# Kernel optimization log

Measured on AMD Instinct MI355X. Metric: run time of the kernel, lower is better.

The kernel has to match this reference:

```python
import jax, jax.numpy as jnp
import numpy as np

K = 16
RADIUS = 1.0
N = 16384
SEQ = 8


def _knn(pc, k):
    """Brute-force kNN of pc against itself. pc: (1, n, 3).
    Returns (dist, idx) each (1, n, k), sorted ascending by distance,
    matching pointutils.knn semantics (Euclidean distance)."""
    x2 = jnp.sum(pc * pc, axis=-1)  # (1, n)
    # d2[b,i,j] = ||p_i - p_j||^2 via expansion; avoids (n,n,3) intermediate
    d2 = x2[:, :, None] + x2[:, None, :] - 2.0 * jnp.einsum('bnd,bmd->bnm', pc, pc)
    d2 = jnp.maximum(d2, 0.0)
    neg_d2, idx = jax.lax.top_k(-d2, k)  # k smallest distances
    dist = jnp.sqrt(jnp.maximum(-neg_d2, 0.0))
    return dist, idx


def setup_inputs() -> dict:
    key = jax.random.key(0)
    k1, k2, k3 = jax.random.split(key, 3)
    return {
        'pc_source': jax.random.normal(k1, (1, N, 3), dtype=jnp.float32),
        'pred_flow': jax.random.normal(k2, (SEQ, N, 3), dtype=jnp.float32),
        'weights': jax.random.uniform(k3, (N,), dtype=jnp.float32),
    }


def reference(pc_source, pred_flow, weights):
    # flow: (seq, 3, n)
    flow = jnp.transpose(pred_flow, (0, 2, 1))
    dist, idx = _knn(pc_source, K)  # (1, n, k)
    # replace out-of-radius neighbors with the nearest (self) index
    idx = jnp.where(dist > RADIUS, idx[:, :, 0:1], idx)
    idx = idx[0]  # (n, k); identical for all sequence steps
    # grouping_operation: gather neighbor flows -> (seq, 3, n, k)
    nn_flow = flow[:, :, idx]
    diff = flow[:, :, :, None] - nn_flow  # (seq, 3, n, k)
    # L2 norm over channel dim (loss_norm=2), safe at 0 (self-neighbor)
    sq = jnp.sum(diff * diff, axis=1)  # (seq, n, k)
    norm = jnp.where(sq > 0, jnp.sqrt(jnp.where(sq > 0, sq, 1.0)), 0.0)
    loss = norm.mean(axis=-1)  # (seq, n)
    loss = loss * weights[None, :]
    loss = loss.sum(axis=1)  # (seq,)
    wsum = weights.sum()
    loss = jnp.where(wsum > 0, loss / wsum, loss)
    return loss.mean()
```

## Files before the change

### kernel.cpp

```cpp
#include <hip/hip_runtime.h>
#include <math.h>

#define NPTS  16384
#define KNN   16
#define SEQV  8
#define NW    16
#define BATCH 8
#define CAPM  15
#define CAPR  1.001f
#define NBKT  256
#define BSCALE 56.8888f
#define HBLK  16

#define SLOT(arr, t, col) arr[(t) * 1024 + (col)]

#define WS_HIST   256
#define WS_STARTS (WS_HIST + NBKT * HBLK * 4)
#define WS_SORTED 18432

__device__ __forceinline__ unsigned umin_(unsigned a, unsigned b) { return a < b ? a : b; }
__device__ __forceinline__ unsigned umax_(unsigned a, unsigned b) { return a > b ? a : b; }

__device__ __forceinline__ int nbucket(float x) { return (int)fminf(x * BSCALE, 255.0f); }

__device__ __forceinline__ void merge_one(unsigned keys[KNN], unsigned kk) {
    if (kk < keys[KNN - 1]) {
#pragma unroll
        for (int u = 0; u < KNN; ++u) {
            unsigned lo = umin_(kk, keys[u]);
            kk = umax_(kk, keys[u]);
            keys[u] = lo;
        }
    }
}

__device__ __forceinline__ void merge16(unsigned k[KNN], const unsigned o[KNN]) {
    unsigned v[KNN];
#pragma unroll
    for (int i = 0; i < KNN; ++i) v[i] = umin_(k[i], o[KNN - 1 - i]);
#pragma unroll
    for (int d = 8; d >= 1; d >>= 1) {
#pragma unroll
        for (int i = 0; i < KNN; ++i) {
            if ((i & d) == 0) {
                unsigned lo = umin_(v[i], v[i + d]);
                unsigned hi = umax_(v[i], v[i + d]);
                v[i] = lo; v[i + d] = hi;
            }
        }
    }
#pragma unroll
    for (int i = 0; i < KNN; ++i) k[i] = v[i];
}

__device__ __forceinline__ void tree_load_merge(unsigned* uS, unsigned keys[KNN], int src) {
    unsigned o[KNN];
#pragma unroll
    for (int t = 0; t < KNN; ++t) o[t] = SLOT(uS, t, src);
    merge16(keys, o);
}

__global__ __launch_bounds__(1024) void hist_kernel(
    const float* __restrict__ pc, unsigned* __restrict__ hist)
{
    __shared__ unsigned h[NBKT];
    const int tid = threadIdx.x;
    if (tid < NBKT) h[tid] = 0u;
    __syncthreads();
    const int i = blockIdx.x * 1024 + tid;
    const float x = pc[3 * i + 0], y = pc[3 * i + 1], z = pc[3 * i + 2];
    const float n = sqrtf(fmaf(x, x, fmaf(y, y, z * z)));
    atomicAdd(&h[nbucket(n)], 1u);
    __syncthreads();
    if (tid < NBKT) hist[tid * HBLK + blockIdx.x] = h[tid];
}

__global__ __launch_bounds__(1024) void scatter_kernel(
    const float* __restrict__ pc, const unsigned* __restrict__ hist,
    unsigned* __restrict__ starts, float* __restrict__ accum,
    float4* __restrict__ sorted4)
{
    __shared__ unsigned sH[NBKT];
    __shared__ unsigned sBase[NBKT];
    __shared__ unsigned sCnt[NBKT];
    const int tid = threadIdx.x;
    const int b   = blockIdx.x;

    unsigned own = 0, pre = 0;
    if (tid < NBKT) {
        const unsigned* row = hist + tid * HBLK;
        unsigned s = 0, p = 0;
#pragma unroll
        for (int k = 0; k < HBLK; ++k) {
            const unsigned c = row[k];
            if (k < b) p += c;
            s += c;
        }
        own = s; pre = p;
        sH[tid] = s;
        sCnt[tid] = 0u;
    }
    __syncthreads();
    for (int off = 1; off < NBKT; off <<= 1) {
        unsigned a = 0u;
        if (tid < NBKT && tid >= off) a = sH[tid - off];
        __syncthreads();
        if (tid < NBKT) sH[tid] += a;
        __syncthreads();
    }
    if (tid < NBKT) {
        const unsigned excl = sH[tid] - own;
        sBase[tid] = excl + pre;
        if (b == 0) starts[tid] = excl;
    }
    if (b == 0 && tid == 0) starts[NBKT] = NPTS;
    if (b == 0 && tid < 8) ((unsigned*)accum)[tid] = 0u;
    __syncthreads();

    const int i = b * 1024 + tid;
    const float x = pc[3 * i + 0], y = pc[3 * i + 1], z = pc[3 * i + 2];
    const float n = sqrtf(fmaf(x, x, fmaf(y, y, z * z)));
    const int bin = nbucket(n);
    const unsigned rank = atomicAdd(&sCnt[bin], 1u);
    sorted4[sBase[bin] + rank] = make_float4(x, y, z, __uint_as_float((unsigned)i));
    if (b == 0 && tid < 8)
        sorted4[NPTS + tid] = make_float4(1e18f, 1e18f, 1e18f, __uint_as_float(0u));
}

__global__ __launch_bounds__(1024, 4) void mega_kernel(
    const float4* __restrict__ sorted, const unsigned* __restrict__ starts,
    const float* __restrict__ flow, const float* __restrict__ wts,
    float* __restrict__ accum, float* __restrict__ out)
{
    __shared__ unsigned uS[1024 * 16];
    float* sred = (float*)&uS[15 * 1024 + 1000];
    float* sTau = (float*)&uS[16320];

    const int tid  = threadIdx.x;
    const int lane = tid & 63;
    const int wv   = __builtin_amdgcn_readfirstlane(tid >> 6);
    const int is   = blockIdx.x * 64 + lane;

    const float4 q4 = sorted[is];
    const float qx = q4.x, qy = q4.y, qz = q4.z;
    const unsigned iorig = __float_as_uint(q4.w);
    const float q2 = fmaf(qx, qx, fmaf(qy, qy, qz * qz));
    const float analytic = 0.19072f * exp2f(0.480898f * q2);
    const float tau0 = fminf(analytic, CAPR);

    const float nq = sqrtf(q2);
    float nmin = nq, nmax = nq;
#pragma unroll
    for (int off = 32; off > 0; off >>= 1) {
        nmin = fminf(nmin, __shfl_xor(nmin, off));
        nmax = fmaxf(nmax, __shfl_xor(nmax, off));
    }
    const float r0 = sqrtf(fminf(0.19072f * exp2f(0.480898f * nmax * nmax), CAPR));
    const int blo = nbucket(fmaxf(nmin - r0, 0.0f));
    const int bhi = nbucket(nmax + r0);
    const int W0  = __builtin_amdgcn_readfirstlane((int)starts[blo]);
    const int W1  = __builtin_amdgcn_readfirstlane((int)starts[bhi + 1]);
    const int nbt = (W1 - W0 + 7) >> 3;

    unsigned keys[KNN];
#pragma unroll
    for (int t = 0; t < KNN; ++t) keys[t] = 0xFFFFFFFFu;
    int cnt = 0;
    unsigned* buf = &uS[tid * CAPM];

    {
        float tauT = tau0;
        const float4* cb = sorted + W0;
        float4 A[BATCH], Bv[BATCH];

        auto procT = [&](const float4* C) {
#pragma unroll
            for (int q = 0; q < BATCH; ++q) {
                const float4 c = C[q];
                float dx = qx - c.x, dy = qy - c.y, dz = qz - c.z;
                float d2 = fmaf(dx, dx, fmaf(dy, dy, dz * dz));
                bool acc = d2 <= tauT;
                if (__any(acc)) {
                    if (acc) {
                        buf[cnt] = (__float_as_uint(d2) & 0xFFFFC000u)
                                 | __float_as_uint(c.w);
                        ++cnt;
                    }
                    if (cnt >= CAPM - 1) {
#pragma unroll 1
                        for (int t = 0; t < cnt; ++t) merge_one(keys, buf[t]);
                        cnt = 0;
                        float d16n = __uint_as_float(keys[KNN - 1] & 0xFFFFC000u);
                        tauT = fminf(tauT, fmaf(d16n, 1.0002f, 1e-6f));
                    }
                }
            }
        };

        int g = wv;
        bool hA = (g < nbt);
        if (hA) { const float4* bp = cb + 8 * g;
#pragma unroll
            for (int q = 0; q < BATCH; ++q) A[q] = bp[q]; }
        while (hA) {
            int g2 = g + 64;
            bool hB = (g2 < nbt);
            if (hB) { const float4* bp = cb + 8 * g2;
#pragma unroll
                for (int q = 0; q < BATCH; ++q) Bv[q] = bp[q]; }
            procT(A);
            if (!hB) break;
            int g3 = g2 + 64;
            bool hC = (g3 < nbt);
            if (hC) { const float4* bp = cb + 8 * g3;
#pragma unroll
                for (int q = 0; q < BATCH; ++q) A[q] = bp[q]; }
            procT(Bv);
            g = g3; hA = hC;
        }
#pragma unroll 1
        for (int t = 0; t < cnt; ++t) merge_one(keys, buf[t]);
        cnt = 0;
    }
    __syncthreads();

#pragma unroll
    for (int t = 0; t < KNN; ++t) SLOT(uS, t, tid) = keys[t];
    __syncthreads();
    if (wv < 8) {
        tree_load_merge(uS, keys, tid + 512);
#pragma unroll
        for (int t = 0; t < KNN; ++t) SLOT(uS, t, tid) = keys[t];
    }
    __syncthreads();
    if (wv < 4) {
        tree_load_merge(uS, keys, tid + 256);
#pragma unroll
        for (int t = 0; t < KNN; ++t) SLOT(uS, t, tid) = keys[t];
    }
    __syncthreads();
    if (wv < 2) {
        tree_load_merge(uS, keys, tid + 128);
#pragma unroll
        for (int t = 0; t < KNN; ++t) SLOT(uS, t, tid) = keys[t];
    }
    __syncthreads();
    if (wv == 0) {
        tree_load_merge(uS, keys, tid + 64);
        const float d16 = __uint_as_float(keys[KNN - 1] & 0xFFFFC000u);
        const float tf  = fmaf(d16, 1.0002f, 1e-6f);
        const bool fail = !(tf <= tau0);
        const float tv = fail ? CAPR : tf;
        sTau[lane] = tv;
        float tm = tv;
#pragma unroll
        for (int off = 32; off > 0; off >>= 1) tm = fmaxf(tm, __shfl_xor(tm, off));
        unsigned long long bw = __ballot(fail && (analytic < CAPR));
        if (lane == 0) { uS[16316] = (bw != 0ull) ? 1u : 0u; ((float*)uS)[16317] = tm; }
    }
    __syncthreads();

    float tauf = sTau[lane];
    const unsigned anyWide = __builtin_amdgcn_readfirstlane(uS[16316]);
    const float rA = sqrtf(((float*)uS)[16317]);
    int W0A, nbtA;
    if (anyWide) { W0A = 0; nbtA = NPTS / 8; }
    else {
        int bloA = nbucket(fmaxf(nmin - rA, 0.0f));
        int bhiA = nbucket(nmax + rA);
        W0A = __builtin_amdgcn_readfirstlane((int)starts[bloA]);
        int W1A = __builtin_amdgcn_readfirstlane((int)starts[bhiA + 1]);
        nbtA = (W1A - W0A + 7) >> 3;
    }
#pragma unroll
    for (int t = 0; t < KNN; ++t) keys[t] = 0xFFFFFFFFu;
    {
        const float4* cb = sorted + W0A;
        float4 A[BATCH], Bv[BATCH];

        auto procA = [&](const float4* C) {
#pragma unroll
            for (int q = 0; q < BATCH; ++q) {
                const float4 c = C[q];
                float dx = qx - c.x, dy = qy - c.y, dz = qz - c.z;
                float d2 = fmaf(dx, dx, fmaf(dy, dy, dz * dz));
                bool acc = d2 <= tauf;
                if (__any(acc)) {
                    if (acc) {
                        buf[cnt] = (__float_as_uint(d2) & 0xFFFFC000u)
                                 | __float_as_uint(c.w);
                        ++cnt;
                    }
                    if (cnt >= CAPM - 1) {
#pragma unroll 1
                        for (int t = 0; t < cnt; ++t) merge_one(keys, buf[t]);
                        cnt = 0;
                        float d16n = __uint_as_float(keys[KNN - 1] & 0xFFFFC000u);
                        tauf = fminf(tauf, fmaf(d16n, 1.0002f, 1e-6f));
                    }
                }
            }
        };

        int g = wv;
        bool hA = (g < nbtA);
        if (hA) { const float4* bp = cb + 8 * g;
#pragma unroll
            for (int q = 0; q < BATCH; ++q) A[q] = bp[q]; }
        while (hA) {
            int g2 = g + 16;
            bool hB = (g2 < nbtA);
            if (hB) { const float4* bp = cb + 8 * g2;
#pragma unroll
                for (int q = 0; q < BATCH; ++q) Bv[q] = bp[q]; }
            procA(A);
            if (!hB) break;
            int g3 = g2 + 16;
            bool hC = (g3 < nbtA);
            if (hC) { const float4* bp = cb + 8 * g3;
#pragma unroll
                for (int q = 0; q < BATCH; ++q) A[q] = bp[q]; }
            procA(Bv);
            g = g3; hA = hC;
        }
#pragma unroll 1
        for (int t = 0; t < cnt; ++t) merge_one(keys, buf[t]);
    }
    __syncthreads();

#pragma unroll
    for (int t = 0; t < KNN; ++t) SLOT(uS, t, tid) = keys[t];
    __syncthreads();
    if (wv < 8) {
        tree_load_merge(uS, keys, tid + 512);
#pragma unroll
        for (int t = 0; t < KNN; ++t) SLOT(uS, t, tid) = keys[t];
    }
    __syncthreads();
    if (wv < 4) {
        tree_load_merge(uS, keys, tid + 256);
#pragma unroll
        for (int t = 0; t < KNN; ++t) SLOT(uS, t, tid) = keys[t];
    }
    __syncthreads();
    if (wv < 2) {
        tree_load_merge(uS, keys, tid + 128);
#pragma unroll
        for (int t = 0; t < KNN; ++t) SLOT(uS, t, tid) = keys[t];
    }
    __syncthreads();
    if (wv == 0) {
        tree_load_merge(uS, keys, tid + 64);
        const int id0 = (int)(keys[0] & 0x3FFFu);
#pragma unroll
        for (int t = 0; t < KNN; ++t) {
            float d2t = __uint_as_float(keys[t] & 0xFFFFC000u);
            int   j   = (int)(keys[t] & 0x3FFFu);
            SLOT(uS, t, lane) = (unsigned)((d2t > 1.0f) ? id0 : j);
        }
    }
    __syncthreads();

    {
        const int s  = wv & 7;
        const int kh = wv >> 3;
        const float* fs = flow + (size_t)s * NPTS * 3;
        const float fx = fs[3 * iorig + 0];
        const float fy = fs[3 * iorig + 1];
        const float fz = fs[3 * iorig + 2];

        float sum = 0.0f;
#pragma unroll
        for (int z = 0; z < 8; ++z) {
            int j = (int)SLOT(uS, kh * 8 + z, lane);
            float dx = fx - fs[3 * j + 0];
            float dy = fy - fs[3 * j + 1];
            float dz = fz - fs[3 * j + 2];
            float sq = fmaf(dx, dx, fmaf(dy, dy, dz * dz));
            sum += (sq > 0.0f) ? sqrtf(sq) : 0.0f;
        }

        float contrib = wts[iorig] * sum;
#pragma unroll
        for (int off = 32; off > 0; off >>= 1) contrib += __shfl_down(contrib, off);
        if (lane == 0) sred[wv] = contrib;

        if (wv == 0) {
            float wi = wts[iorig];
#pragma unroll
            for (int off = 32; off > 0; off >>= 1) wi += __shfl_down(wi, off);
            if (lane == 0) atomicAdd(&accum[1], wi);
        }
        __syncthreads();

        if (tid == 0) {
            float c = 0.0f;
#pragma unroll
            for (int t = 0; t < NW; ++t) c += sred[t];
            atomicAdd(&accum[0], c);
            __threadfence();
            unsigned ticket = atomicAdd((unsigned*)accum + 2, 1u);
            if (ticket == gridDim.x - 1) {
                float a  = atomicAdd(&accum[0], 0.0f);
                float ws = atomicAdd(&accum[1], 0.0f);
                float v  = a / (float)(KNN * SEQV);
                out[0] = (ws > 0.0f) ? (v / ws) : v;
            }
        }
    }
}

extern "C" void kernel_launch(void* const* d_in, const int* in_sizes, int n_in,
                              void* d_out, int out_size, void* d_ws, size_t ws_size,
                              hipStream_t stream)
{
    const float* pc   = (const float*)d_in[0];
    const float* flow = (const float*)d_in[1];
    const float* wts  = (const float*)d_in[2];
    float* out = (float*)d_out;

    float*    accum  = (float*)d_ws;
    unsigned* hist   = (unsigned*)((char*)d_ws + WS_HIST);
    unsigned* starts = (unsigned*)((char*)d_ws + WS_STARTS);
    float4*   sorted = (float4*)  ((char*)d_ws + WS_SORTED);

    hist_kernel   <<<HBLK, 1024, 0, stream>>>(pc, hist);
    scatter_kernel<<<HBLK, 1024, 0, stream>>>(pc, hist, starts, accum, sorted);
    mega_kernel   <<<NPTS / 64, 1024, 0, stream>>>(sorted, starts, flow, wts, accum, out);
}
```

Measured before the change: 150.9 us.

## Split each query group across two blocks and precompute distance expansion terms

Each 64-query group is now handled by two blocks, each scanning alternating 8-candidate chunks. A global counter lets the second finishing block merge both partial top-16 lists through a workspace buffer, then run the flow loss. Candidates are stored as (-2x,-2y,-2z,|c|^2) with indices in a separate array, so each distance test is three FMAs against a shifted threshold. This doubles the grid to raise parallelism, at the cost of duplicated threshold setup, global key traffic, an extra merge and an extra index load per candidate.

Measured after the change: 180.5 us. +19.6%, slower.

```diff
diff --git a/kernel.cpp b/kernel.cpp
--- a/kernel.cpp
+++ b/kernel.cpp
@@ -11,12 +11,16 @@
 #define NBKT  256
 #define BSCALE 56.8888f
 #define HBLK  16
+#define NGRP  256
 
 #define SLOT(arr, t, col) arr[(t) * 1024 + (col)]
 
 #define WS_HIST   256
-#define WS_STARTS (WS_HIST + NBKT * HBLK * 4)
-#define WS_SORTED 18432
+#define WS_STARTS 16640
+#define WS_GCTR   17920
+#define WS_SIDX   18944
+#define WS_SORTED 84480
+#define WS_KEYB   346752
 
 __device__ __forceinline__ unsigned umin_(unsigned a, unsigned b) { return a < b ? a : b; }
 __device__ __forceinline__ unsigned umax_(unsigned a, unsigned b) { return a > b ? a : b; }
@@ -77,7 +81,8 @@
 
 __global__ __launch_bounds__(1024) void scatter_kernel(
     const float* __restrict__ pc, const unsigned* __restrict__ hist,
-    unsigned* __restrict__ starts, float* __restrict__ accum,
+    unsigned* __restrict__ starts, unsigned* __restrict__ gctr,
+    float* __restrict__ accum, unsigned* __restrict__ sidx,
     float4* __restrict__ sorted4)
 {
     __shared__ unsigned sH[NBKT];
@@ -111,7 +116,7 @@
     if (tid < NBKT) {
         const unsigned excl = sH[tid] - own;
         sBase[tid] = excl + pre;
-        if (b == 0) starts[tid] = excl;
+        if (b == 0) { starts[tid] = excl; gctr[tid] = 0u; }
     }
     if (b == 0 && tid == 0) starts[NBKT] = NPTS;
     if (b == 0 && tid < 8) ((unsigned*)accum)[tid] = 0u;
@@ -119,18 +124,25 @@
 
     const int i = b * 1024 + tid;
     const float x = pc[3 * i + 0], y = pc[3 * i + 1], z = pc[3 * i + 2];
-    const float n = sqrtf(fmaf(x, x, fmaf(y, y, z * z)));
+    const float c2 = fmaf(x, x, fmaf(y, y, z * z));
+    const float n = sqrtf(c2);
     const int bin = nbucket(n);
     const unsigned rank = atomicAdd(&sCnt[bin], 1u);
-    sorted4[sBase[bin] + rank] = make_float4(x, y, z, __uint_as_float((unsigned)i));
-    if (b == 0 && tid < 8)
-        sorted4[NPTS + tid] = make_float4(1e18f, 1e18f, 1e18f, __uint_as_float(0u));
+    const unsigned pos = sBase[bin] + rank;
+    sorted4[pos] = make_float4(-2.0f * x, -2.0f * y, -2.0f * z, c2);
+    sidx[pos] = (unsigned)i;
+    if (b == 0 && tid < 8) {
+        sorted4[NPTS + tid] = make_float4(0.0f, 0.0f, 0.0f, 1e18f);
+        sidx[NPTS + tid] = 0u;
+    }
 }
 
 __global__ __launch_bounds__(1024, 4) void mega_kernel(
-    const float4* __restrict__ sorted, const unsigned* __restrict__ starts,
+    const float4* __restrict__ sorted, const unsigned* __restrict__ sidx,
+    const unsigned* __restrict__ starts, unsigned* __restrict__ gctr,
     const float* __restrict__ flow, const float* __restrict__ wts,
-    float* __restrict__ accum, float* __restrict__ out)
+    float* __restrict__ accum, unsigned* __restrict__ keybuf,
+    float* __restrict__ out)
 {
     __shared__ unsigned uS[1024 * 16];
     float* sred = (float*)&uS[15 * 1024 + 1000];
@@ -139,12 +151,16 @@
     const int tid  = threadIdx.x;
     const int lane = tid & 63;
     const int wv   = __builtin_amdgcn_readfirstlane(tid >> 6);
-    const int is   = blockIdx.x * 64 + lane;
-
-    const float4 q4 = sorted[is];
-    const float qx = q4.x, qy = q4.y, qz = q4.z;
-    const unsigned iorig = __float_as_uint(q4.w);
-    const float q2 = fmaf(qx, qx, fmaf(qy, qy, qz * qz));
+    const int g    = blockIdx.x >> 1;
+    const int h    = blockIdx.x & 1;
+    const int is   = g * 64 + lane;
+
+    const float4 mi = sorted[is];
+    const float qx = -0.5f * mi.x;
+    const float qy = -0.5f * mi.y;
+    const float qz = -0.5f * mi.z;
+    const float q2 = mi.w;
+    const unsigned iorig = sidx[is];
     const float analytic = 0.19072f * exp2f(0.480898f * q2);
     const float tau0 = fminf(analytic, CAPR);
 
@@ -158,9 +174,8 @@
     const float r0 = sqrtf(fminf(0.19072f * exp2f(0.480898f * nmax * nmax), CAPR));
     const int blo = nbucket(fmaxf(nmin - r0, 0.0f));
     const int bhi = nbucket(nmax + r0);
-    const int W0  = __builtin_amdgcn_readfirstlane((int)starts[blo]);
-    const int W1  = __builtin_amdgcn_readfirstlane((int)starts[bhi + 1]);
-    const int nbt = (W1 - W0 + 7) >> 3;
+    const int k0  = __builtin_amdgcn_readfirstlane((int)starts[blo]) >> 3;
+    const int ke  = (__builtin_amdgcn_readfirstlane((int)starts[bhi + 1]) + 7) >> 3;
 
     unsigned keys[KNN];
 #pragma unroll
@@ -169,21 +184,20 @@
     unsigned* buf = &uS[tid * CAPM];
 
     {
-        float tauT = tau0;
-        const float4* cb = sorted + W0;
+        float taufs = tau0 - q2;
         float4 A[BATCH], Bv[BATCH];
-
-        auto procT = [&](const float4* C) {
+        unsigned As[BATCH], Bs[BATCH];
+
+        auto proc = [&](const float4* C, const unsigned* S) {
 #pragma unroll
             for (int q = 0; q < BATCH; ++q) {
                 const float4 c = C[q];
-                float dx = qx - c.x, dy = qy - c.y, dz = qz - c.z;
-                float d2 = fmaf(dx, dx, fmaf(dy, dy, dz * dz));
-                bool acc = d2 <= tauT;
+                float d2p = fmaf(c.x, qx, fmaf(c.y, qy, fmaf(c.z, qz, c.w)));
+                bool acc = d2p <= taufs;
                 if (__any(acc)) {
                     if (acc) {
-                        buf[cnt] = (__float_as_uint(d2) & 0xFFFFC000u)
-                                 | __float_as_uint(c.w);
+                        float d2 = fmaxf(d2p + q2, 0.0f);
+                        buf[cnt] = (__float_as_uint(d2) & 0xFFFFC000u) | S[q];
                         ++cnt;
                     }
                     if (cnt >= CAPM - 1) {
@@ -191,32 +205,31 @@
                         for (int t = 0; t < cnt; ++t) merge_one(keys, buf[t]);
                         cnt = 0;
                         float d16n = __uint_as_float(keys[KNN - 1] & 0xFFFFC000u);
-                        tauT = fminf(tauT, fmaf(d16n, 1.0002f, 1e-6f));
+                        taufs = fminf(taufs, fmaf(d16n, 1.0002f, 1e-6f) - q2);
                     }
                 }
             }
         };
 
-        int g = wv;
-        bool hA = (g < nbt);
-        if (hA) { const float4* bp = cb + 8 * g;
-#pragma unroll
-            for (int q = 0; q < BATCH; ++q) A[q] = bp[q]; }
+        const int tb = k0 + ((k0 ^ h) & 1);
+        int k = tb + 2 * wv;
+        bool hA = (k < ke);
+        if (hA) { const float4* bp = sorted + (k << 3); const unsigned* sp = sidx + (k << 3);
+#pragma unroll
+            for (int q = 0; q < BATCH; ++q) { A[q] = bp[q]; As[q] = sp[q]; } }
         while (hA) {
-            int g2 = g + 64;
-            bool hB = (g2 < nbt);
-            if (hB) { const float4* bp = cb + 8 * g2;
-#pragma unroll
-                for (int q = 0; q < BATCH; ++q) Bv[q] = bp[q]; }
-            procT(A);
+            int k2 = k + 64; bool hB = (k2 < ke);
+            if (hB) { const float4* bp = sorted + (k2 << 3); const unsigned* sp = sidx + (k2 << 3);
+#pragma unroll
+                for (int q = 0; q < BATCH; ++q) { Bv[q] = bp[q]; Bs[q] = sp[q]; } }
+            proc(A, As);
             if (!hB) break;
-            int g3 = g2 + 64;
-            bool hC = (g3 < nbt);
-            if (hC) { const float4* bp = cb + 8 * g3;
-#pragma unroll
-                for (int q = 0; q < BATCH; ++q) A[q] = bp[q]; }
-            procT(Bv);
-            g = g3; hA = hC;
+            int k3 = k2 + 64; bool hC = (k3 < ke);
+            if (hC) { const float4* bp = sorted + (k3 << 3); const unsigned* sp = sidx + (k3 << 3);
+#pragma unroll
+                for (int q = 0; q < BATCH; ++q) { A[q] = bp[q]; As[q] = sp[q]; } }
+            proc(Bv, Bs);
+            k = k3; hA = hC;
         }
 #pragma unroll 1
         for (int t = 0; t < cnt; ++t) merge_one(keys, buf[t]);
@@ -260,35 +273,33 @@
     }
     __syncthreads();
 
-    float tauf = sTau[lane];
+    float taufs = sTau[lane] - q2;
     const unsigned anyWide = __builtin_amdgcn_readfirstlane(uS[16316]);
     const float rA = sqrtf(((float*)uS)[16317]);
-    int W0A, nbtA;
-    if (anyWide) { W0A = 0; nbtA = NPTS / 8; }
+    int kA0, kAe;
+    if (anyWide) { kA0 = 0; kAe = NPTS / 8; }
     else {
         int bloA = nbucket(fmaxf(nmin - rA, 0.0f));
         int bhiA = nbucket(nmax + rA);
-        W0A = __builtin_amdgcn_readfirstlane((int)starts[bloA]);
-        int W1A = __builtin_amdgcn_readfirstlane((int)starts[bhiA + 1]);
-        nbtA = (W1A - W0A + 7) >> 3;
+        kA0 = __builtin_amdgcn_readfirstlane((int)starts[bloA]) >> 3;
+        kAe = (__builtin_amdgcn_readfirstlane((int)starts[bhiA + 1]) + 7) >> 3;
     }
 #pragma unroll
     for (int t = 0; t < KNN; ++t) keys[t] = 0xFFFFFFFFu;
     {
-        const float4* cb = sorted + W0A;
         float4 A[BATCH], Bv[BATCH];
-
-        auto procA = [&](const float4* C) {
+        unsigned As[BATCH], Bs[BATCH];
+
+        auto proc = [&](const float4* C, const unsigned* S) {
 #pragma unroll
             for (int q = 0; q < BATCH; ++q) {
                 const float4 c = C[q];
-                float dx = qx - c.x, dy = qy - c.y, dz = qz - c.z;
-                float d2 = fmaf(dx, dx, fmaf(dy, dy, dz * dz));
-                bool acc = d2 <= tauf;
+                float d2p = fmaf(c.x, qx, fmaf(c.y, qy, fmaf(c.z, qz, c.w)));
+                bool acc = d2p <= taufs;
                 if (__any(acc)) {
                     if (acc) {
-                        buf[cnt] = (__float_as_uint(d2) & 0xFFFFC000u)
-                                 | __float_as_uint(c.w);
+                        float d2 = fmaxf(d2p + q2, 0.0f);
+                        buf[cnt] = (__float_as_uint(d2) & 0xFFFFC000u) | S[q];
                         ++cnt;
                     }
                     if (cnt >= CAPM - 1) {
@@ -296,32 +307,31 @@
                         for (int t = 0; t < cnt; ++t) merge_one(keys, buf[t]);
                         cnt = 0;
                         float d16n = __uint_as_float(keys[KNN - 1] & 0xFFFFC000u);
-                        tauf = fminf(tauf, fmaf(d16n, 1.0002f, 1e-6f));
+                        taufs = fminf(taufs, fmaf(d16n, 1.0002f, 1e-6f) - q2);
                     }
                 }
             }
         };
 
-        int g = wv;
-        bool hA = (g < nbtA);
-        if (hA) { const float4* bp = cb + 8 * g;
-#pragma unroll
-            for (int q = 0; q < BATCH; ++q) A[q] = bp[q]; }
+        const int ab = kA0 + ((kA0 ^ h) & 1);
+        int k = ab + 2 * wv;
+        bool hA = (k < kAe);
+        if (hA) { const float4* bp = sorted + (k << 3); const unsigned* sp = sidx + (k << 3);
+#pragma unroll
+            for (int q = 0; q < BATCH; ++q) { A[q] = bp[q]; As[q] = sp[q]; } }
         while (hA) {
-            int g2 = g + 16;
-            bool hB = (g2 < nbtA);
-            if (hB) { const float4* bp = cb + 8 * g2;
-#pragma unroll
-                for (int q = 0; q < BATCH; ++q) Bv[q] = bp[q]; }
-            procA(A);
+            int k2 = k + 32; bool hB = (k2 < kAe);
+            if (hB) { const float4* bp = sorted + (k2 << 3); const unsigned* sp = sidx + (k2 << 3);
+#pragma unroll
+                for (int q = 0; q < BATCH; ++q) { Bv[q] = bp[q]; Bs[q] = sp[q]; } }
+            proc(A, As);
             if (!hB) break;
-            int g3 = g2 + 16;
-            bool hC = (g3 < nbtA);
-            if (hC) { const float4* bp = cb + 8 * g3;
-#pragma unroll
-                for (int q = 0; q < BATCH; ++q) A[q] = bp[q]; }
-            procA(Bv);
-            g = g3; hA = hC;
+            int k3 = k2 + 32; bool hC = (k3 < kAe);
+            if (hC) { const float4* bp = sorted + (k3 << 3); const unsigned* sp = sidx + (k3 << 3);
+#pragma unroll
+                for (int q = 0; q < BATCH; ++q) { A[q] = bp[q]; As[q] = sp[q]; } }
+            proc(Bv, Bs);
+            k = k3; hA = hC;
         }
 #pragma unroll 1
         for (int t = 0; t < cnt; ++t) merge_one(keys, buf[t]);
@@ -351,6 +361,26 @@
     __syncthreads();
     if (wv == 0) {
         tree_load_merge(uS, keys, tid + 64);
+        unsigned* kb = keybuf + ((size_t)(2 * g + h) << 10);
+#pragma unroll
+        for (int t = 0; t < KNN; ++t) kb[t * 64 + lane] = keys[t];
+    }
+    __syncthreads();
+
+    if (tid == 0) {
+        __threadfence();
+        uS[16316] = atomicAdd(&gctr[g], 1u);
+    }
+    __syncthreads();
+    if (uS[16316] == 0u) return;
+
+    if (wv == 0) {
+        unsigned o[KNN];
+        unsigned* kbo = keybuf + ((size_t)(2 * g + (h ^ 1)) << 10);
+#pragma unroll
+        for (int t = 0; t < KNN; ++t)
+            o[t] = atomicAdd(&kbo[t * 64 + lane], 0u);
+        merge16(keys, o);
         const int id0 = (int)(keys[0] & 0x3FFFu);
 #pragma unroll
         for (int t = 0; t < KNN; ++t) {
@@ -400,7 +430,7 @@
             atomicAdd(&accum[0], c);
             __threadfence();
             unsigned ticket = atomicAdd((unsigned*)accum + 2, 1u);
-            if (ticket == gridDim.x - 1) {
+            if (ticket == NGRP - 1) {
                 float a  = atomicAdd(&accum[0], 0.0f);
                 float ws = atomicAdd(&accum[1], 0.0f);
                 float v  = a / (float)(KNN * SEQV);
@@ -422,9 +452,13 @@
     float*    accum  = (float*)d_ws;
     unsigned* hist   = (unsigned*)((char*)d_ws + WS_HIST);
     unsigned* starts = (unsigned*)((char*)d_ws + WS_STARTS);
+    unsigned* gctr   = (unsigned*)((char*)d_ws + WS_GCTR);
+    unsigned* sidx   = (unsigned*)((char*)d_ws + WS_SIDX);
     float4*   sorted = (float4*)  ((char*)d_ws + WS_SORTED);
+    unsigned* keybuf = (unsigned*)((char*)d_ws + WS_KEYB);
 
     hist_kernel   <<<HBLK, 1024, 0, stream>>>(pc, hist);
-    scatter_kernel<<<HBLK, 1024, 0, stream>>>(pc, hist, starts, accum, sorted);
-    mega_kernel   <<<NPTS / 64, 1024, 0, stream>>>(sorted, starts, flow, wts, accum, out);
-}
+    scatter_kernel<<<HBLK, 1024, 0, stream>>>(pc, hist, starts, gctr, accum, sidx, sorted);
+    mega_kernel   <<<2 * NGRP, 1024, 0, stream>>>(sorted, sidx, starts, gctr,
+                                                  flow, wts, accum, keybuf, out);
+}
```
